# Performance work log

Measured on AMD Instinct MI355X. Metric: run time of the kernel, lower is better.

## Reference

```python
import jax, jax.numpy as jnp
import numpy as np
import math

B, CZ, L = 1, 128, 256
H, C = 4, 32  # num_heads, head dim
EPS = 1e-5


def _conv1x1(w, x):
    # w: (out, in), x: (b, in, i, j) -> (b, out, i, j)
    return jnp.einsum('oc,bcij->boij', w, x)


def setup_inputs() -> dict:
    key = jax.random.key(0)
    ks = jax.random.split(key, 8)
    s = 1.0 / math.sqrt(CZ)
    return {
        'pair_rep': jax.random.normal(ks[0], (B, CZ, L, L), jnp.float32),
        'ln_gamma': jnp.ones((CZ, L, L), jnp.float32),
        'ln_beta': jnp.zeros((CZ, L, L), jnp.float32),
        'w_q': jax.random.normal(ks[1], (H * C, CZ), jnp.float32) * s,
        'w_k': jax.random.normal(ks[2], (H * C, CZ), jnp.float32) * s,
        'w_v': jax.random.normal(ks[3], (H * C, CZ), jnp.float32) * s,
        'w_b': jax.random.normal(ks[4], (H, CZ), jnp.float32) * s,
        'w_g': jax.random.normal(ks[5], (H * C, CZ), jnp.float32) * s,
        'b_g': jnp.zeros((H * C,), jnp.float32),
        'w_rep': jax.random.normal(ks[6], (CZ, H * C), jnp.float32) * s,
        'b_rep': jnp.zeros((CZ,), jnp.float32),
    }


def reference(pair_rep, ln_gamma, ln_beta, w_q, w_k, w_v, w_b, w_g, b_g, w_rep, b_rep):
    # LayerNorm over (c_z, h, w) jointly, full-shape affine (torch LayerNorm([c_z,h,w]))
    mu = jnp.mean(pair_rep, axis=(1, 2, 3), keepdims=True)
    var = jnp.var(pair_rep, axis=(1, 2, 3), keepdims=True)
    x = (pair_rep - mu) * jax.lax.rsqrt(var + EPS) * ln_gamma[None] + ln_beta[None]

    # 1x1 conv projections; channels packed as (h c): channel = h*C + c
    q = _conv1x1(w_q, x).reshape(B, H, C, L, L)  # bhcij
    k = _conv1x1(w_k, x).reshape(B, H, C, L, L)
    v = _conv1x1(w_v, x).reshape(B, H, C, L, L)
    bias = _conv1x1(w_b, x)                       # (b, h, i, j) -> used as bias[b,h,j,k]
    g = jax.nn.sigmoid(_conv1x1(w_g, x) + b_g[None, :, None, None]).reshape(B, H, C, L, L)

    scale = 1.0 / math.sqrt(C)
    # scores[b,h,i,j,k] = scale * sum_c q[b,h,c,i,j] k[b,h,c,i,k] + bias[b,h,j,k]
    scores = scale * jnp.einsum('bhcij,bhcik->bhijk', q, k) + bias[:, :, None, :, :]
    a = jax.nn.softmax(scores, axis=-1)
    # o[b,h,c,i,j] = sum_k a[b,h,i,j,k] v[b,h,c,i,k]  (same math as the 6D broadcast-sum)
    o = g * jnp.einsum('bhijk,bhcik->bhcij', a, v)

    # output repacks channels as (c h): channel = c*H + h
    o = jnp.transpose(o, (0, 2, 1, 3, 4)).reshape(B, C * H, L, L)
    return _conv1x1(w_rep, o) + b_rep[None, :, None, None]
```

## Files before the change

### kernel.cpp

```cpp
#include <hip/hip_runtime.h>
#include <math.h>

#define L 256
#define CZ 128
#define NH 4
#define HD 32
#define P (L*L)
#define NTOT (CZ*P)
#define EPSV 1e-5f
#define SCALE 0.17677669529663687f

typedef unsigned short u16;
typedef _Float16 f16;
typedef __attribute__((ext_vector_type(8))) _Float16 f16x8;
typedef __attribute__((ext_vector_type(4))) _Float16 f16x4;
typedef __attribute__((ext_vector_type(4))) float    f32x4;

__device__ __forceinline__ float bu2f(u16 u){ return __uint_as_float(((unsigned)u) << 16); }
__device__ __forceinline__ u16 f2bu(float x){
  unsigned u = __float_as_uint(x);
  return (u16)((u + 0x7fffu + ((u >> 16) & 1u)) >> 16);
}

template<bool FP32>
__device__ __forceinline__ float ldin(const void* p, size_t i){
  return FP32 ? ((const float*)p)[i] : bu2f(((const u16*)p)[i]);
}
template<bool FP32>
__device__ __forceinline__ void stout(void* p, size_t i, float v){
  if (FP32) ((float*)p)[i] = v; else ((u16*)p)[i] = f2bu(v);
}

__device__ __forceinline__ void glds16(const void* g, void* l){
  __builtin_amdgcn_global_load_lds((const __attribute__((address_space(1))) void*)g,
                                   (__attribute__((address_space(3))) void*)l, 16, 0, 0);
}

#define OFF_WQT   16
#define OFF_WKT   (OFF_WQT+16384)
#define OFF_WVT   (OFF_WKT+16384)
#define OFF_WGT   (OFF_WVT+16384)
#define OFF_WREPT (OFF_WGT+16384)
#define OFF_WBT   (OFF_WREPT+16384)
#define OFF_BGF   (OFF_WBT+512)
#define OFF_BREPF (OFF_BGF+128)
#define OFF_BIAS  (OFF_BREPF+128)
#define OFF_XN    344848
#define OFF_ATTO  (OFF_XN+4194304)
#define WS_NEED   (((size_t)OFF_ATTO + 4194304ull)*4ull)

#define GUARD(ws) if (((((const volatile int*)(ws))[2]) != 0) != FP32) return;

__global__ __launch_bounds__(256) void detect_dtype(const void* pair, int* flag){
  int t = threadIdx.x;
  const u16* u = (const u16*)pair;
  int big = 0;
  for (int k = t; k < 2048; k += 256){
    float av = fabsf(bu2f(u[k]));
    if (!(av < 1e4f)) big = 1;
  }
  __shared__ int sb[256];
  sb[t] = big; __syncthreads();
  for (int off = 128; off > 0; off >>= 1){
    if (t < off) sb[t] |= sb[t+off];
    __syncthreads();
  }
  if (t == 0) flag[2] = sb[0];
}

template<bool FP32>
__global__ __launch_bounds__(256) void prep_w(const void* wq, const void* wk,
    const void* wv, const void* wg, const void* wrep, const void* wb,
    const void* bg, const void* brep, float* ws){
  GUARD(ws);
  int idx = blockIdx.x*256 + threadIdx.x;
  int oc = idx >> 7, cin = idx & 127;
  f16* wf = (f16*)(ws + OFF_WQT);
  wf[0*16384 + idx] = (f16)ldin<FP32>(wq, idx);
  wf[1*16384 + idx] = (f16)ldin<FP32>(wk, idx);
  wf[2*16384 + idx] = (f16)ldin<FP32>(wv, idx);
  wf[3*16384 + idx] = (f16)ldin<FP32>(wg, idx);
  float wr = ldin<FP32>(wrep, idx);
  ws[OFF_WREPT + cin*128 + oc] = wr;
  ((f16*)(ws + OFF_WVT))[oc*128 + (cin&3)*32 + (cin>>2)] = (f16)wr;
  if (idx < 512){ int h = idx >> 7, ci = idx & 127; ws[OFF_WBT + ci*4 + h] = ldin<FP32>(wb, idx); }
  if (idx < 128){ ws[OFF_BGF + idx] = ldin<FP32>(bg, idx); ws[OFF_BREPF + idx] = ldin<FP32>(brep, idx); }
}

template<bool FP32>
__global__ __launch_bounds__(256) void ln_reduce(const void* __restrict__ pair, float* ws){
  GUARD(ws);
  int t = threadIdx.x;
  int g = blockIdx.x*256 + t;
  float s = 0.f, ss = 0.f;
  #pragma unroll
  for (int u = 0; u < 4; ++u){
    size_t vi = (size_t)u*524288 + g;
    if (FP32){
      float4 v = ((const float4*)pair)[vi];
      s += v.x+v.y+v.z+v.w;
      ss += v.x*v.x + v.y*v.y + v.z*v.z + v.w*v.w;
    } else {
      ushort4 v = ((const ushort4*)pair)[vi];
      float a = bu2f(v.x), b = bu2f(v.y), c = bu2f(v.z), d = bu2f(v.w);
      s += a+b+c+d; ss += a*a+b*b+c*c+d*d;
    }
  }
  __shared__ float sa[256], sb[256];
  sa[t] = s; sb[t] = ss;
  __syncthreads();
  for (int off = 128; off > 0; off >>= 1){
    if (t < off){ sa[t] += sa[t+off]; sb[t] += sb[t+off]; }
    __syncthreads();
  }
  if (t == 0){ atomicAdd(&ws[0], sa[0]); atomicAdd(&ws[1], sb[0]); }
}


template<bool FP32>
__global__ __launch_bounds__(256) void xnorm(const void* __restrict__ pair,
    const void* __restrict__ gamma, const void* __restrict__ beta, float* __restrict__ ws){
  GUARD(ws);
  int a = blockIdx.x & 255, q = blockIdx.x >> 8;
  int t = threadIdx.x;
  int cq = t >> 6, b64 = t & 63, j4 = b64 << 2;
  float mu   = ws[0] * (1.0f/NTOT);
  float var  = ws[1] * (1.0f/NTOT) - mu*mu;
  float rstd = rsqrtf(var + EPSV);
  f16 hv[4][8];
  #pragma unroll
  for (int ce = 0; ce < 8; ++ce){
    int c = q*32 + cq*8 + ce;
    size_t vi = (size_t)c*16384 + (size_t)a*64 + b64;
    float p0,p1,p2,p3, g0,g1,g2,g3, e0,e1,e2,e3;
    if (FP32){
      float4 pv = ((const float4*)pair)[vi];
      float4 gv = ((const float4*)gamma)[vi];
      float4 bv = ((const float4*)beta)[vi];
      p0=pv.x;p1=pv.y;p2=pv.z;p3=pv.w; g0=gv.x;g1=gv.y;g2=gv.z;g3=gv.w; e0=bv.x;e1=bv.y;e2=bv.z;e3=bv.w;
    } else {
      ushort4 pv = ((const ushort4*)pair)[vi];
      ushort4 gv = ((const ushort4*)gamma)[vi];
      ushort4 bv = ((const ushort4*)beta)[vi];
      p0=bu2f(pv.x);p1=bu2f(pv.y);p2=bu2f(pv.z);p3=bu2f(pv.w);
      g0=bu2f(gv.x);g1=bu2f(gv.y);g2=bu2f(gv.z);g3=bu2f(gv.w);
      e0=bu2f(bv.x);e1=bu2f(bv.y);e2=bu2f(bv.z);e3=bu2f(bv.w);
    }
    hv[0][ce] = (f16)((p0-mu)*rstd*g0 + e0);
    hv[1][ce] = (f16)((p1-mu)*rstd*g1 + e1);
    hv[2][ce] = (f16)((p2-mu)*rstd*g2 + e2);
    hv[3][ce] = (f16)((p3-mu)*rstd*g3 + e3);
  }
  char* xnb = (char*)ws + (size_t)OFF_XN*4;
  int cb = q*4 + cq;
  #pragma unroll
  for (int col = 0; col < 4; ++col){
    f16x8 v;
    #pragma unroll
    for (int ce = 0; ce < 8; ++ce) v[ce] = hv[col][ce];
    *(f16x8*)(xnb + ((((size_t)a*16 + cb)*256) + (j4+col))*16) = v;
  }
}

__global__ __launch_bounds__(256) void bias_xn(float* __restrict__ ws){
  int a = blockIdx.x & 255, qc = blockIdx.x >> 8, b = threadIdx.x;
  const char* xnb = (const char*)ws + (size_t)OFF_XN*4;
  float a0=0.f, a1=0.f, a2=0.f, a3=0.f;
  #pragma unroll
  for (int cc = 0; cc < 4; ++cc){
    int cb = qc*4 + cc;
    f16x8 v = *(const f16x8*)(xnb + ((((size_t)a*16 + cb)*256) + b)*16);
    #pragma unroll
    for (int ce = 0; ce < 8; ++ce){
      int c = cb*8 + ce;
      float xv = (float)v[ce];
      const float* w4 = ws + OFF_WBT + c*4;
      a0 = fmaf(w4[0], xv, a0); a1 = fmaf(w4[1], xv, a1);
      a2 = fmaf(w4[2], xv, a2); a3 = fmaf(w4[3], xv, a3);
    }
  }
  atomicAdd(&ws[OFF_BIAS + 0*P + a*L + b], a0);
  atomicAdd(&ws[OFF_BIAS + 1*P + a*L + b], a1);
  atomicAdd(&ws[OFF_BIAS + 2*P + a*L + b], a2);
  atomicAdd(&ws[OFF_BIAS + 3*P + a*L + b], a3);
}

__global__ __launch_bounds__(256, 4) void attn_xn(float* __restrict__ ws){
  __shared__ __align__(16) char smem[32768];
  char* Ab = smem;
  char* Bb = smem + 16384;
  const int t = threadIdx.x;
  int bid = blockIdx.x;
  int sw = ((bid & 7) << 7) | (bid >> 3);
  const int h = sw >> 8, i = sw & 255;
  const int w = t >> 6, l = t & 63;
  const int l15 = l & 15, l4 = l >> 4;
  const char* xnb = (const char*)ws + (size_t)OFF_XN*4 + (size_t)i*65536;
  const f16* wf = (const f16*)(ws + OFF_WQT);

  auto stage = [&](int q){
    #pragma unroll
    for (int cbl = 0; cbl < 4; ++cbl){
      int jsrc = (w*64 + l) ^ cbl;
      const char* src = xnb + (size_t)((q*4 + cbl)*4096) + (size_t)jsrc*16;
      glds16(src, Ab + cbl*4096 + w*1024);
    }
  };

  f32x4 acc[2][4][2];
  auto projpass = [&](int pr0){
    #pragma unroll
    for (int pp = 0; pp < 2; ++pp)
      #pragma unroll
      for (int mj = 0; mj < 4; ++mj)
        #pragma unroll
        for (int nt = 0; nt < 2; ++nt) acc[pp][mj][nt] = f32x4{0.f,0.f,0.f,0.f};
    #pragma unroll
    for (int q = 0; q < 4; ++q){
      __syncthreads();
      f16x8 A[4];
      #pragma unroll
      for (int mj = 0; mj < 4; ++mj){
        int j = 64*w + 16*mj + l15;
        A[mj] = *(const f16x8*)(Ab + l4*4096 + ((j ^ l4)*16));
      }
      __syncthreads();
      if (q < 3) stage(q+1);
      #pragma unroll
      for (int pp = 0; pp < 2; ++pp){
        #pragma unroll
        for (int nt = 0; nt < 2; ++nt){
          int o = h*32 + nt*16 + l15;
          f16x8 Bf = *(const f16x8*)(wf + (pr0+pp)*16384 + o*128 + q*32 + 8*l4);
          #pragma unroll
          for (int mj = 0; mj < 4; ++mj)
            acc[pp][mj][nt] = __builtin_amdgcn_mfma_f32_16x16x32_f16(A[mj], Bf, acc[pp][mj][nt], 0, 0, 0);
        }
      }
    }
  };

  stage(0);
  projpass(0);
  __syncthreads();
  stage(0);
  #pragma unroll
  for (int mj = 0; mj < 4; ++mj){
    #pragma unroll
    for (int nt = 0; nt < 2; ++nt){
      int ob = 2*nt + (l15 >> 3), oe = l15 & 7;
      int kb4 = 64*w + 16*mj + 4*l4;
      #pragma unroll
      for (int r = 0; r < 4; ++r)
        *(f16*)(Bb + ((ob*4096 + (kb4+r)*16 + oe*2) ^ ((ob&3)<<4))) = (f16)acc[0][mj][nt][r];
    }
  }
  __syncthreads();
  f16x8 qa[4];
  #pragma unroll
  for (int mj = 0; mj < 4; ++mj){
    int j = 64*w + 16*mj + l15;
    qa[mj] = *(const f16x8*)(Bb + ((l4*4096 + j*16) ^ ((l4&3)<<4)));
  }
  __syncthreads();
  #pragma unroll
  for (int mj = 0; mj < 4; ++mj){
    #pragma unroll
    for (int nt = 0; nt < 2; ++nt){
      int ob = 2*nt + (l15 >> 3), oe = l15 & 7;
      int kb4 = 64*w + 16*mj + 4*l4;
      #pragma unroll
      for (int r = 0; r < 4; ++r)
        *(f16*)(Bb + ((ob*4096 + (kb4+r)*16 + oe*2) ^ ((ob&3)<<4))) = (f16)acc[1][mj][nt][r];
    }
  }

  projpass(2);
  f16x4 gsh[4][2];
  #pragma unroll
  for (int mj = 0; mj < 4; ++mj){
    #pragma unroll
    for (int nt = 0; nt < 2; ++nt){
      float bgv = ws[OFF_BGF + h*32 + nt*16 + l15];
      #pragma unroll
      for (int r = 0; r < 4; ++r){
        float z = acc[1][mj][nt][r] + bgv;
        gsh[mj][nt][r] = (f16)(1.0f/(1.0f + __expf(-z)));
      }
    }
  }
  __syncthreads();
  #pragma unroll
  for (int mj = 0; mj < 4; ++mj){
    #pragma unroll
    for (int nt = 0; nt < 2; ++nt){
      int c = nt*16 + l15;
      int kkq = 16*w + 4*mj + l4;
      f16x4 pv;
      #pragma unroll
      for (int r = 0; r < 4; ++r) pv[r] = (f16)acc[0][mj][nt][r];
      *(f16x4*)(Ab + kkq*256 + ((c*8) ^ (l4<<3))) = pv;
    }
  }
  __syncthreads();

  f32x4 oacc[4][2];
  #pragma unroll
  for (int mj = 0; mj < 4; ++mj)
    #pragma unroll
    for (int nt = 0; nt < 2; ++nt) oacc[mj][nt] = f32x4{0.f,0.f,0.f,0.f};
  float lp[4] = {0.f,0.f,0.f,0.f};
  const float* bias2 = ws + OFF_BIAS + (size_t)h*P;
  const f32x4 zz = {0.f,0.f,0.f,0.f};

  for (int kt = 0; kt < 8; ++kt){
    int kk0 = kt*32, kkq0 = kt*8;
    f16x8 kbf[2];
    #pragma unroll
    for (int tt = 0; tt < 2; ++tt)
      kbf[tt] = *(const f16x8*)(Bb + ((l4*4096 + (kk0+16*tt+l15)*16) ^ ((l4&3)<<4)));
    f16x4 vb[2][2];
    #pragma unroll
    for (int tt = 0; tt < 2; ++tt)
      #pragma unroll
      for (int nt = 0; nt < 2; ++nt)
        vb[tt][nt] = *(const f16x4*)(Ab + (kkq0+4*tt+l4)*256 + ((((l15+16*nt)*8)) ^ (l4<<3)));
    #pragma unroll
    for (int mj = 0; mj < 4; ++mj){
      int j = 64*w + 16*mj + l15;
      const float* bp = bias2 + (size_t)j*256 + kk0 + 4*l4;
      #pragma unroll
      for (int tt = 0; tt < 2; ++tt){
        f32x4 s = __builtin_amdgcn_mfma_f32_16x16x32_f16(kbf[tt], qa[mj], zz, 0, 0, 0);
        float4 bv = *(const float4*)(bp + 16*tt);
        f16x4 pa;
        {
          float e0 = __expf(fmaf(s[0], SCALE, bv.x - 4.0f));
          float e1 = __expf(fmaf(s[1], SCALE, bv.y - 4.0f));
          float e2 = __expf(fmaf(s[2], SCALE, bv.z - 4.0f));
          float e3 = __expf(fmaf(s[3], SCALE, bv.w - 4.0f));
          lp[mj] += (e0+e1)+(e2+e3);
          pa[0]=(f16)e0; pa[1]=(f16)e1; pa[2]=(f16)e2; pa[3]=(f16)e3;
        }
        #pragma unroll
        for (int nt = 0; nt < 2; ++nt)
          oacc[mj][nt] = __builtin_amdgcn_mfma_f32_16x16x16f16(pa, vb[tt][nt], oacc[mj][nt], 0, 0, 0);
      }
    }
  }

  float inv[4];
  #pragma unroll
  for (int mj = 0; mj < 4; ++mj){
    float v = lp[mj];
    v += __shfl_xor(v, 16);
    v += __shfl_xor(v, 32);
    inv[mj] = 1.0f / v;
  }
  __syncthreads();
  #pragma unroll
  for (int mj = 0; mj < 4; ++mj){
    #pragma unroll
    for (int r = 0; r < 4; ++r){
      float iv = __shfl(inv[mj], 20*l4 + r);
      int j = 64*w + 16*mj + 4*l4 + r;
      #pragma unroll
      for (int nt = 0; nt < 2; ++nt){
        int c = nt*16 + l15;
        float ov = oacc[mj][nt][r] * iv * (float)gsh[mj][nt][r];
        *(f16*)(Bb + c*512 + ((j*2) ^ ((c&7)<<4))) = (f16)ov;
      }
    }
  }
  __syncthreads();
  char* ao = (char*)ws + (size_t)OFF_ATTO*4;
  #pragma unroll
  for (int cb8 = 0; cb8 < 4; ++cb8){
    f16x8 v;
    #pragma unroll
    for (int e = 0; e < 8; ++e){
      int c = cb8*8 + e;
      v[e] = *(const f16*)(Bb + c*512 + ((t*2) ^ ((c&7)<<4)));
    }
    *(f16x8*)(ao + (((size_t)i*256 + t)*128 + h*32)*2 + cb8*16) = v;
  }
}

template<bool FP32>
__global__ __launch_bounds__(256, 4) void out_proj_mf(float* __restrict__ ws, void* __restrict__ outp){
  GUARD(ws);
  __shared__ __align__(16) char smem[32768];
  char* Ab = smem;
  char* Ob = smem + 16384;
  const int t = threadIdx.x;
  int bid = blockIdx.x;
  int sw2 = ((bid & 7) << 6) | (bid >> 3);
  const int oh = sw2 >> 8, i = sw2 & 255;
  const int w = t >> 6, l = t & 63;
  const int l15 = l & 15, l4 = l >> 4;
  const char* aob = (const char*)ws + (size_t)OFF_ATTO*4 + (size_t)i*65536;
  const f16* w2 = (const f16*)(ws + OFF_WVT);

  auto stage = [&](int q){
    #pragma unroll
    for (int cbl = 0; cbl < 4; ++cbl){
      int jsrc = (w*64 + l) ^ cbl;
      const char* src = aob + (size_t)jsrc*256 + (q*4 + cbl)*16;
      glds16(src, Ab + cbl*4096 + w*1024);
    }
  };

  f32x4 acc[4][4];
  #pragma unroll
  for (int nt = 0; nt < 4; ++nt)
    #pragma unroll
    for (int mj = 0; mj < 4; ++mj) acc[nt][mj] = f32x4{0.f,0.f,0.f,0.f};

  stage(0);
  #pragma unroll
  for (int q = 0; q < 4; ++q){
    __syncthreads();
    f16x8 A[4];
    #pragma unroll
    for (int mj = 0; mj < 4; ++mj){
      int j = 64*w + 16*mj + l15;
      A[mj] = *(const f16x8*)(Ab + l4*4096 + ((j ^ l4)*16));
    }
    __syncthreads();
    if (q < 3) stage(q+1);
    #pragma unroll
    for (int nt = 0; nt < 4; ++nt){
      int oc = oh*64 + nt*16 + l15;
      f16x8 Bf = *(const f16x8*)(w2 + oc*128 + q*32 + 8*l4);
      #pragma unroll
      for (int mj = 0; mj < 4; ++mj)
        acc[nt][mj] = __builtin_amdgcn_mfma_f32_16x16x32_f16(A[mj], Bf, acc[nt][mj], 0, 0, 0);
    }
  }
  #pragma unroll
  for (int nt = 0; nt < 4; ++nt){
    __syncthreads();
    #pragma unroll
    for (int mj = 0; mj < 4; ++mj){
      #pragma unroll
      for (int r = 0; r < 4; ++r){
        int j = 64*w + 16*mj + 4*l4 + r;
        *(float*)(Ob + l15*1024 + ((j*4) ^ ((l15&7)<<4))) = acc[nt][mj][r];
      }
    }
    __syncthreads();
    #pragma unroll
    for (int o2 = 0; o2 < 16; ++o2){
      int oc = oh*64 + nt*16 + o2;
      float v = *(const float*)(Ob + o2*1024 + ((t*4) ^ ((o2&7)<<4)));
      stout<FP32>(outp, (size_t)oc*P + (size_t)i*L + t, v + ws[OFF_BREPF + oc]);
    }
  }
}


template<bool FP32>
__global__ __launch_bounds__(256) void bias_old(const void* __restrict__ pair,
    const void* __restrict__ gamma, const void* __restrict__ beta, float* __restrict__ ws){
  GUARD(ws);
  int a = blockIdx.x & 255, q = blockIdx.x >> 8, b = threadIdx.x;
  float mu   = ws[0] * (1.0f/NTOT);
  float var  = ws[1] * (1.0f/NTOT) - mu*mu;
  float rstd = rsqrtf(var + EPSV);
  float a0=0.f, a1=0.f, a2=0.f, a3=0.f;
  int c0 = q*32;
  for (int cc = 0; cc < 32; ++cc){
    int c = c0 + cc;
    size_t idx = (size_t)c*P + (size_t)a*L + b;
    float xv = (ldin<FP32>(pair,idx) - mu)*rstd*ldin<FP32>(gamma,idx) + ldin<FP32>(beta,idx);
    const float* w4 = ws + OFF_WBT + c*4;
    a0 = fmaf(w4[0], xv, a0); a1 = fmaf(w4[1], xv, a1);
    a2 = fmaf(w4[2], xv, a2); a3 = fmaf(w4[3], xv, a3);
  }
  atomicAdd(&ws[OFF_BIAS + 0*P + a*L + b], a0);
  atomicAdd(&ws[OFF_BIAS + 1*P + a*L + b], a1);
  atomicAdd(&ws[OFF_BIAS + 2*P + a*L + b], a2);
  atomicAdd(&ws[OFF_BIAS + 3*P + a*L + b], a3);
}

template<bool FP32>
__global__ __launch_bounds__(256, 2) void attn_old(const void* __restrict__ pair,
    const void* __restrict__ gamma, const void* __restrict__ beta,
    float* __restrict__ ws, void* __restrict__ outp){
  GUARD(ws);
  __shared__ __align__(16) char smem[65536];
  char* Ab  = smem;
  char* KTb = smem + 32768;
  char* V2b = smem + 49152;
  const int t = threadIdx.x;
  const int h = blockIdx.x >> 8, i = blockIdx.x & 255;
  const int w = t >> 6, l = t & 63;
  const int l15 = l & 15, l4 = l >> 4;
  const float mu   = ws[0] * (1.0f/NTOT);
  const float var  = ws[1] * (1.0f/NTOT) - mu*mu;
  const float rstd = rsqrtf(var + EPSV);
  const f16* wf = (const f16*)(ws + OFF_WQT);
  f32x4 acc[4][4][2];
  #pragma unroll
  for (int pr=0;pr<4;++pr)
    #pragma unroll
    for(int mj=0;mj<4;++mj)
      #pragma unroll
      for(int nt=0;nt<2;++nt) acc[pr][mj][nt] = f32x4{0.f,0.f,0.f,0.f};
  for (int half = 0; half < 2; ++half){
    #pragma unroll
    for (int cb = 0; cb < 8; ++cb){
      int cc0 = cb*8;
      f16x8 hv;
      #pragma unroll
      for (int e = 0; e < 8; ++e){
        size_t idx = (size_t)(half*64 + cc0 + e)*P + (size_t)i*L + t;
        float xv = (ldin<FP32>(pair,idx) - mu)*rstd*ldin<FP32>(gamma,idx) + ldin<FP32>(beta,idx);
        hv[e] = (f16)xv;
      }
      *(f16x8*)(Ab + t*128 + ((cc0*2) ^ ((t&7)<<4))) = hv;
    }
    __syncthreads();
    #pragma unroll
    for (int ksl = 0; ksl < 2; ++ksl){
      int cin0 = half*64 + ksl*32;
      f16x8 A[4];
      #pragma unroll
      for (int mj = 0; mj < 4; ++mj){
        int j = 64*w + 16*mj + l15;
        A[mj] = *(const f16x8*)(Ab + j*128 + (((ksl*32 + 8*l4)*2) ^ ((j&7)<<4)));
      }
      #pragma unroll
      for (int pr = 0; pr < 4; ++pr){
        #pragma unroll
        for (int nt = 0; nt < 2; ++nt){
          int o = h*32 + nt*16 + l15;
          f16x8 Bf = *(const f16x8*)(wf + pr*16384 + o*128 + cin0 + 8*l4);
          #pragma unroll
          for (int mj = 0; mj < 4; ++mj)
            acc[pr][mj][nt] = __builtin_amdgcn_mfma_f32_16x16x32_f16(A[mj], Bf, acc[pr][mj][nt], 0, 0, 0);
        }
      }
    }
    __syncthreads();
  }
  f32x4 gs[4][2];
  #pragma unroll
  for (int mj = 0; mj < 4; ++mj){
    #pragma unroll
    for (int nt = 0; nt < 2; ++nt){
      float bgv = ws[OFF_BGF + h*32 + nt*16 + l15];
      #pragma unroll
      for (int r = 0; r < 4; ++r){
        float z = acc[3][mj][nt][r] + bgv;
        gs[mj][nt][r] = 1.0f/(1.0f + __expf(-z));
      }
    }
  }
  #pragma unroll
  for (int mj = 0; mj < 4; ++mj){
    #pragma unroll
    for (int nt = 0; nt < 2; ++nt){
      int o = nt*16 + l15;
      int kb4 = 64*w + 16*mj + 4*l4;
      f16x4 pv;
      #pragma unroll
      for (int r = 0; r < 4; ++r){
        int j = kb4 + r;
        *(f16*)(Ab  + j*64 + ((o*2) ^ ((j&3)<<4))) = (f16)acc[0][mj][nt][r];
        *(f16*)(KTb + j*64 + ((o*2) ^ ((j&3)<<4))) = (f16)acc[1][mj][nt][r];
        pv[r] = (f16)acc[2][mj][nt][r];
      }
      *(f16x4*)(V2b + o*512 + ((kb4*2) ^ ((o&7)<<4))) = pv;
    }
  }
  __syncthreads();
  f16x8 qa[4];
  #pragma unroll
  for (int mj = 0; mj < 4; ++mj){
    int j = 64*w + 16*mj + l15;
    qa[mj] = *(const f16x8*)(Ab + j*64 + ((16*l4) ^ ((j&3)<<4)));
  }
  __syncthreads();
  f32x4 oacc[4][2];
  #pragma unroll
  for (int mj=0;mj<4;++mj)
    #pragma unroll
    for(int nt=0;nt<2;++nt) oacc[mj][nt] = f32x4{0.f,0.f,0.f,0.f};
  float lp[16];
  #pragma unroll
  for (int u = 0; u < 16; ++u) lp[u] = 0.f;
  const float* bias2 = ws + OFF_BIAS + (size_t)h*P;
  const f32x4 zz = {0.f,0.f,0.f,0.f};
  for (int kt = 0; kt < 4; ++kt){
    int kk0 = kt*64;
    #pragma unroll
    for (int nk = 0; nk < 4; ++nk){
      int kkr = kk0 + nk*16 + l15;
      f16x8 kbf = *(const f16x8*)(KTb + kkr*64 + ((16*l4) ^ ((kkr&3)<<4)));
      #pragma unroll
      for (int mj = 0; mj < 4; ++mj){
        f32x4 s = __builtin_amdgcn_mfma_f32_16x16x32_f16(qa[mj], kbf, zz, 0, 0, 0);
        #pragma unroll
        for (int r = 0; r < 4; ++r){
          int j = 64*w + 16*mj + 4*l4 + r;
          float bv = bias2[(size_t)j*L + kkr] - 4.0f;
          float e = __expf(fmaf(s[r], SCALE, bv));
          lp[mj*4+r] += e;
          *(f16*)(Ab + j*128 + (((nk*16+l15)*2) ^ ((j&7)<<4))) = (f16)e;
        }
      }
    }
    __syncthreads();
    #pragma unroll
    for (int ks2 = 0; ks2 < 2; ++ks2){
      f16x8 vb[2];
      #pragma unroll
      for (int nt = 0; nt < 2; ++nt){
        int c = nt*16 + l15;
        vb[nt] = *(const f16x8*)(V2b + c*512 + (((kk0 + ks2*32 + 8*l4)*2) ^ ((c&7)<<4)));
      }
      #pragma unroll
      for (int mj = 0; mj < 4; ++mj){
        int j = 64*w + 16*mj + l15;
        f16x8 pa = *(const f16x8*)(Ab + j*128 + (((ks2*32 + 8*l4)*2) ^ ((j&7)<<4)));
        #pragma unroll
        for (int nt = 0; nt < 2; ++nt)
          oacc[mj][nt] = __builtin_amdgcn_mfma_f32_16x16x32_f16(pa, vb[nt], oacc[mj][nt], 0, 0, 0);
      }
    }
  }
  __syncthreads();
  #pragma unroll
  for (int u = 0; u < 16; ++u){
    float v = lp[u];
    v += __shfl_xor(v, 1);
    v += __shfl_xor(v, 2);
    v += __shfl_xor(v, 4);
    v += __shfl_xor(v, 8);
    lp[u] = 1.0f / v;
  }
  #pragma unroll
  for (int mj = 0; mj < 4; ++mj){
    #pragma unroll
    for (int nt = 0; nt < 2; ++nt){
      int c = nt*16 + l15;
      #pragma unroll
      for (int r = 0; r < 4; ++r){
        int j = 64*w + 16*mj + 4*l4 + r;
        float ov = oacc[mj][nt][r] * lp[mj*4+r] * gs[mj][nt][r];
        *(float*)(Ab + c*1024 + ((j*4) ^ ((c&7)<<4))) = ov;
      }
    }
  }
  __syncthreads();
  #pragma unroll
  for (int c = 0; c < 32; ++c){
    float v = *(const float*)(Ab + c*1024 + ((t*4) ^ ((c&7)<<4)));
    stout<FP32>(outp, (size_t)(c*NH + h)*P + (size_t)i*L + t, v);
  }
}

template<bool FP32>
__global__ __launch_bounds__(256) void out_proj_old(float* __restrict__ ws, void* __restrict__ outp){
  GUARD(ws);
  __shared__ float gos[CZ*65];
  int blk = blockIdx.x;
  int i = blk >> 2, jb = (blk & 3) << 6;
  int t = threadIdx.x;
  for (int u = 0; u < 32; ++u){
    int lin = u*256 + t;
    int m = lin >> 6, p = lin & 63;
    gos[m*65 + p] = ldin<FP32>(outp, (size_t)m*P + (size_t)i*L + jb + p);
  }
  __syncthreads();
  int p = t & 63, w4 = t >> 6;
  int woc = w4*32;
  float acc[32];
  #pragma unroll
  for (int o = 0; o < 32; ++o) acc[o] = 0.f;
  for (int cin = 0; cin < CZ; ++cin){
    float xv = gos[cin*65 + p];
    const float* wrow = ws + OFF_WREPT + cin*128 + woc;
    #pragma unroll
    for (int o = 0; o < 32; ++o) acc[o] = fmaf(wrow[o], xv, acc[o]);
  }
  #pragma unroll
  for (int o = 0; o < 32; ++o){
    int oc = woc + o;
    stout<FP32>(outp, (size_t)oc*P + (size_t)i*L + jb + p, acc[o] + ws[OFF_BREPF + oc]);
  }
}

extern "C" void kernel_launch(void* const* d_in, const int* in_sizes, int n_in,
                              void* d_out, int out_size, void* d_ws, size_t ws_size,
                              hipStream_t stream) {
  (void)in_sizes; (void)n_in; (void)out_size;
  const void* pair  = d_in[0];
  const void* gamma = d_in[1];
  const void* beta  = d_in[2];
  const void* wq    = d_in[3];
  const void* wk    = d_in[4];
  const void* wv    = d_in[5];
  const void* wb    = d_in[6];
  const void* wg    = d_in[7];
  const void* bg    = d_in[8];
  const void* wrep  = d_in[9];
  const void* brep  = d_in[10];
  float* ws = (float*)d_ws;
  bool big = ws_size >= WS_NEED;

  hipMemsetAsync(d_ws, 0, 16, stream);
  hipMemsetAsync((char*)d_ws + (size_t)OFF_BIAS*4, 0, (size_t)NH*P*4, stream);
  detect_dtype<<<1, 256, 0, stream>>>(pair, (int*)d_ws);

  prep_w<false>   <<<64,   256, 0, stream>>>(wq, wk, wv, wg, wrep, wb, bg, brep, ws);
  prep_w<true>    <<<64,   256, 0, stream>>>(wq, wk, wv, wg, wrep, wb, bg, brep, ws);
  ln_reduce<false><<<2048, 256, 0, stream>>>(pair, ws);
  ln_reduce<true> <<<2048, 256, 0, stream>>>(pair, ws);

  if (big){
    xnorm<false>       <<<1024, 256, 0, stream>>>(pair, gamma, beta, ws);
    xnorm<true>        <<<1024, 256, 0, stream>>>(pair, gamma, beta, ws);
    bias_xn            <<<1024, 256, 0, stream>>>(ws);
    attn_xn            <<<1024, 256, 0, stream>>>(ws);
    out_proj_mf<false> <<<512,  256, 0, stream>>>(ws, d_out);
    out_proj_mf<true>  <<<512,  256, 0, stream>>>(ws, d_out);
  } else {
    bias_old<false>    <<<1024, 256, 0, stream>>>(pair, gamma, beta, ws);
    bias_old<true>     <<<1024, 256, 0, stream>>>(pair, gamma, beta, ws);
    attn_old<false>    <<<1024, 256, 0, stream>>>(pair, gamma, beta, ws, d_out);
    attn_old<true>     <<<1024, 256, 0, stream>>>(pair, gamma, beta, ws, d_out);
    out_proj_old<false><<<1024, 256, 0, stream>>>(ws, d_out);
    out_proj_old<true> <<<1024, 256, 0, stream>>>(ws, d_out);
  }
}
```

Before: 330.3 us.

## Fuse bias projection into xnorm, drop dual-dtype launches, relayout attention output

The separate bias_xn pass is folded into xnorm: each block accumulates the per-head bias projection from fp32 normalized values, reduces it through shared memory and atomically adds it, with the softmax offset of -4 folded into the stored bias instead of being applied in attn_xn. The templated FP32/BF16 kernel pairs, which each launched twice and returned early on a guard, become single kernels that branch on the runtime dtype flag, removing several launches. attn_xn now preloads bias tiles ahead of the MFMA loop, and the attention output is stored head-major so out_proj_mf can stage it contiguously. out_proj_mf uses 1024 blocks of 32 output channels instead of 512 blocks of 64, trading weight and A-tile reuse for more parallelism.

```diff
diff --git a/kernel.cpp b/kernel.cpp
--- a/kernel.cpp
+++ b/kernel.cpp
@@ -22,6 +22,12 @@
   return (u16)((u + 0x7fffu + ((u >> 16) & 1u)) >> 16);
 }
 
+__device__ __forceinline__ float ldr(bool fp32, const void* p, size_t i){
+  return fp32 ? ((const float*)p)[i] : bu2f(((const u16*)p)[i]);
+}
+__device__ __forceinline__ void str(bool fp32, void* p, size_t i, float v){
+  if (fp32) ((float*)p)[i] = v; else ((u16*)p)[i] = f2bu(v);
+}
 template<bool FP32>
 __device__ __forceinline__ float ldin(const void* p, size_t i){
   return FP32 ? ((const float*)p)[i] : bu2f(((const u16*)p)[i]);
@@ -50,6 +56,7 @@
 #define WS_NEED   (((size_t)OFF_ATTO + 4194304ull)*4ull)
 
 #define GUARD(ws) if (((((const volatile int*)(ws))[2]) != 0) != FP32) return;
+#define RFLAG(ws) (((const volatile int*)(ws))[2] != 0)
 
 __global__ __launch_bounds__(256) void detect_dtype(const void* pair, int* flag){
   int t = threadIdx.x;
@@ -68,40 +75,40 @@
   if (t == 0) flag[2] = sb[0];
 }
 
-template<bool FP32>
 __global__ __launch_bounds__(256) void prep_w(const void* wq, const void* wk,
     const void* wv, const void* wg, const void* wrep, const void* wb,
     const void* bg, const void* brep, float* ws){
-  GUARD(ws);
+  bool fp32 = RFLAG(ws);
   int idx = blockIdx.x*256 + threadIdx.x;
   int oc = idx >> 7, cin = idx & 127;
   f16* wf = (f16*)(ws + OFF_WQT);
-  wf[0*16384 + idx] = (f16)ldin<FP32>(wq, idx);
-  wf[1*16384 + idx] = (f16)ldin<FP32>(wk, idx);
-  wf[2*16384 + idx] = (f16)ldin<FP32>(wv, idx);
-  wf[3*16384 + idx] = (f16)ldin<FP32>(wg, idx);
-  float wr = ldin<FP32>(wrep, idx);
+  wf[0*16384 + idx] = (f16)ldr(fp32, wq, idx);
+  wf[1*16384 + idx] = (f16)ldr(fp32, wk, idx);
+  wf[2*16384 + idx] = (f16)ldr(fp32, wv, idx);
+  wf[3*16384 + idx] = (f16)ldr(fp32, wg, idx);
+  float wr = ldr(fp32, wrep, idx);
   ws[OFF_WREPT + cin*128 + oc] = wr;
   ((f16*)(ws + OFF_WVT))[oc*128 + (cin&3)*32 + (cin>>2)] = (f16)wr;
-  if (idx < 512){ int h = idx >> 7, ci = idx & 127; ws[OFF_WBT + ci*4 + h] = ldin<FP32>(wb, idx); }
-  if (idx < 128){ ws[OFF_BGF + idx] = ldin<FP32>(bg, idx); ws[OFF_BREPF + idx] = ldin<FP32>(brep, idx); }
-}
-
-template<bool FP32>
+  if (idx < 512){ int h = idx >> 7, ci = idx & 127; ws[OFF_WBT + ci*4 + h] = ldr(fp32, wb, idx); }
+  if (idx < 128){ ws[OFF_BGF + idx] = ldr(fp32, bg, idx); ws[OFF_BREPF + idx] = ldr(fp32, brep, idx); }
+}
+
 __global__ __launch_bounds__(256) void ln_reduce(const void* __restrict__ pair, float* ws){
-  GUARD(ws);
+  bool fp32 = RFLAG(ws);
   int t = threadIdx.x;
   int g = blockIdx.x*256 + t;
   float s = 0.f, ss = 0.f;
-  #pragma unroll
-  for (int u = 0; u < 4; ++u){
-    size_t vi = (size_t)u*524288 + g;
-    if (FP32){
-      float4 v = ((const float4*)pair)[vi];
+  if (fp32){
+    #pragma unroll
+    for (int u = 0; u < 4; ++u){
+      float4 v = ((const float4*)pair)[(size_t)u*524288 + g];
       s += v.x+v.y+v.z+v.w;
       ss += v.x*v.x + v.y*v.y + v.z*v.z + v.w*v.w;
-    } else {
-      ushort4 v = ((const ushort4*)pair)[vi];
+    }
+  } else {
+    #pragma unroll
+    for (int u = 0; u < 4; ++u){
+      ushort4 v = ((const ushort4*)pair)[(size_t)u*524288 + g];
       float a = bu2f(v.x), b = bu2f(v.y), c = bu2f(v.z), d = bu2f(v.w);
       s += a+b+c+d; ss += a*a+b*b+c*c+d*d;
     }
@@ -117,10 +124,9 @@
 }
 
 
-template<bool FP32>
 __global__ __launch_bounds__(256) void xnorm(const void* __restrict__ pair,
     const void* __restrict__ gamma, const void* __restrict__ beta, float* __restrict__ ws){
-  GUARD(ws);
+  bool fp32 = RFLAG(ws);
   int a = blockIdx.x & 255, q = blockIdx.x >> 8;
   int t = threadIdx.x;
   int cq = t >> 6, b64 = t & 63, j4 = b64 << 2;
@@ -128,12 +134,17 @@
   float var  = ws[1] * (1.0f/NTOT) - mu*mu;
   float rstd = rsqrtf(var + EPSV);
   f16 hv[4][8];
+  float pb[4][4];
+  #pragma unroll
+  for (int col = 0; col < 4; ++col)
+    #pragma unroll
+    for (int h = 0; h < 4; ++h) pb[col][h] = 0.f;
   #pragma unroll
   for (int ce = 0; ce < 8; ++ce){
     int c = q*32 + cq*8 + ce;
     size_t vi = (size_t)c*16384 + (size_t)a*64 + b64;
     float p0,p1,p2,p3, g0,g1,g2,g3, e0,e1,e2,e3;
-    if (FP32){
+    if (fp32){
       float4 pv = ((const float4*)pair)[vi];
       float4 gv = ((const float4*)gamma)[vi];
       float4 bv = ((const float4*)beta)[vi];
@@ -146,10 +157,20 @@
       g0=bu2f(gv.x);g1=bu2f(gv.y);g2=bu2f(gv.z);g3=bu2f(gv.w);
       e0=bu2f(bv.x);e1=bu2f(bv.y);e2=bu2f(bv.z);e3=bu2f(bv.w);
     }
-    hv[0][ce] = (f16)((p0-mu)*rstd*g0 + e0);
-    hv[1][ce] = (f16)((p1-mu)*rstd*g1 + e1);
-    hv[2][ce] = (f16)((p2-mu)*rstd*g2 + e2);
-    hv[3][ce] = (f16)((p3-mu)*rstd*g3 + e3);
+    float x0 = (p0-mu)*rstd*g0 + e0;
+    float x1 = (p1-mu)*rstd*g1 + e1;
+    float x2 = (p2-mu)*rstd*g2 + e2;
+    float x3 = (p3-mu)*rstd*g3 + e3;
+    hv[0][ce] = (f16)x0; hv[1][ce] = (f16)x1; hv[2][ce] = (f16)x2; hv[3][ce] = (f16)x3;
+    float4 w4 = *(const float4*)(ws + OFF_WBT + c*4);
+    pb[0][0] = fmaf(w4.x, x0, pb[0][0]); pb[0][1] = fmaf(w4.y, x0, pb[0][1]);
+    pb[0][2] = fmaf(w4.z, x0, pb[0][2]); pb[0][3] = fmaf(w4.w, x0, pb[0][3]);
+    pb[1][0] = fmaf(w4.x, x1, pb[1][0]); pb[1][1] = fmaf(w4.y, x1, pb[1][1]);
+    pb[1][2] = fmaf(w4.z, x1, pb[1][2]); pb[1][3] = fmaf(w4.w, x1, pb[1][3]);
+    pb[2][0] = fmaf(w4.x, x2, pb[2][0]); pb[2][1] = fmaf(w4.y, x2, pb[2][1]);
+    pb[2][2] = fmaf(w4.z, x2, pb[2][2]); pb[2][3] = fmaf(w4.w, x2, pb[2][3]);
+    pb[3][0] = fmaf(w4.x, x3, pb[3][0]); pb[3][1] = fmaf(w4.y, x3, pb[3][1]);
+    pb[3][2] = fmaf(w4.z, x3, pb[3][2]); pb[3][3] = fmaf(w4.w, x3, pb[3][3]);
   }
   char* xnb = (char*)ws + (size_t)OFF_XN*4;
   int cb = q*4 + cq;
@@ -160,29 +181,20 @@
     for (int ce = 0; ce < 8; ++ce) v[ce] = hv[col][ce];
     *(f16x8*)(xnb + ((((size_t)a*16 + cb)*256) + (j4+col))*16) = v;
   }
-}
-
-__global__ __launch_bounds__(256) void bias_xn(float* __restrict__ ws){
-  int a = blockIdx.x & 255, qc = blockIdx.x >> 8, b = threadIdx.x;
-  const char* xnb = (const char*)ws + (size_t)OFF_XN*4;
-  float a0=0.f, a1=0.f, a2=0.f, a3=0.f;
-  #pragma unroll
-  for (int cc = 0; cc < 4; ++cc){
-    int cb = qc*4 + cc;
-    f16x8 v = *(const f16x8*)(xnb + ((((size_t)a*16 + cb)*256) + b)*16);
-    #pragma unroll
-    for (int ce = 0; ce < 8; ++ce){
-      int c = cb*8 + ce;
-      float xv = (float)v[ce];
-      const float* w4 = ws + OFF_WBT + c*4;
-      a0 = fmaf(w4[0], xv, a0); a1 = fmaf(w4[1], xv, a1);
-      a2 = fmaf(w4[2], xv, a2); a3 = fmaf(w4[3], xv, a3);
-    }
-  }
-  atomicAdd(&ws[OFF_BIAS + 0*P + a*L + b], a0);
-  atomicAdd(&ws[OFF_BIAS + 1*P + a*L + b], a1);
-  atomicAdd(&ws[OFF_BIAS + 2*P + a*L + b], a2);
-  atomicAdd(&ws[OFF_BIAS + 3*P + a*L + b], a3);
+  __shared__ float sbb[4][64][16];
+  #pragma unroll
+  for (int col = 0; col < 4; ++col)
+    #pragma unroll
+    for (int h = 0; h < 4; ++h) sbb[cq][b64][h*4+col] = pb[col][h];
+  __syncthreads();
+  #pragma unroll
+  for (int k = 0; k < 4; ++k){
+    int lin = k*256 + t;
+    int bb = lin >> 4, hc = lin & 15;
+    float v = sbb[0][bb][hc] + sbb[1][bb][hc] + sbb[2][bb][hc] + sbb[3][bb][hc];
+    int h = hc >> 2, col = hc & 3;
+    atomicAdd(&ws[OFF_BIAS + h*P + a*256 + bb*4 + col], v - 1.0f);
+  }
 }
 
 __global__ __launch_bounds__(256, 4) void attn_xn(float* __restrict__ ws){
@@ -315,6 +327,13 @@
 
   for (int kt = 0; kt < 8; ++kt){
     int kk0 = kt*32, kkq0 = kt*8;
+    float4 bvv[4][2];
+    #pragma unroll
+    for (int mj = 0; mj < 4; ++mj){
+      const float* bp = bias2 + (size_t)(64*w + 16*mj + l15)*256 + kk0 + 4*l4;
+      bvv[mj][0] = *(const float4*)bp;
+      bvv[mj][1] = *(const float4*)(bp + 16);
+    }
     f16x8 kbf[2];
     #pragma unroll
     for (int tt = 0; tt < 2; ++tt)
@@ -327,18 +346,16 @@
         vb[tt][nt] = *(const f16x4*)(Ab + (kkq0+4*tt+l4)*256 + ((((l15+16*nt)*8)) ^ (l4<<3)));
     #pragma unroll
     for (int mj = 0; mj < 4; ++mj){
-      int j = 64*w + 16*mj + l15;
-      const float* bp = bias2 + (size_t)j*256 + kk0 + 4*l4;
       #pragma unroll
       for (int tt = 0; tt < 2; ++tt){
         f32x4 s = __builtin_amdgcn_mfma_f32_16x16x32_f16(kbf[tt], qa[mj], zz, 0, 0, 0);
-        float4 bv = *(const float4*)(bp + 16*tt);
+        float4 bv = bvv[mj][tt];
         f16x4 pa;
         {
-          float e0 = __expf(fmaf(s[0], SCALE, bv.x - 4.0f));
-          float e1 = __expf(fmaf(s[1], SCALE, bv.y - 4.0f));
-          float e2 = __expf(fmaf(s[2], SCALE, bv.z - 4.0f));
-          float e3 = __expf(fmaf(s[3], SCALE, bv.w - 4.0f));
+          float e0 = __expf(fmaf(s[0], SCALE, bv.x));
+          float e1 = __expf(fmaf(s[1], SCALE, bv.y));
+          float e2 = __expf(fmaf(s[2], SCALE, bv.z));
+          float e3 = __expf(fmaf(s[3], SCALE, bv.w));
           lp[mj] += (e0+e1)+(e2+e3);
           pa[0]=(f16)e0; pa[1]=(f16)e1; pa[2]=(f16)e2; pa[3]=(f16)e3;
         }
@@ -373,7 +390,7 @@
     }
   }
   __syncthreads();
-  char* ao = (char*)ws + (size_t)OFF_ATTO*4;
+  char* ao = (char*)ws + (size_t)OFF_ATTO*4 + (size_t)h*4194304 + ((size_t)i*256)*64;
   #pragma unroll
   for (int cb8 = 0; cb8 < 4; ++cb8){
     f16x8 v;
@@ -382,37 +399,36 @@
       int c = cb8*8 + e;
       v[e] = *(const f16*)(Bb + c*512 + ((t*2) ^ ((c&7)<<4)));
     }
-    *(f16x8*)(ao + (((size_t)i*256 + t)*128 + h*32)*2 + cb8*16) = v;
-  }
-}
-
-template<bool FP32>
+    *(f16x8*)(ao + (size_t)t*64 + cb8*16) = v;
+  }
+}
+
 __global__ __launch_bounds__(256, 4) void out_proj_mf(float* __restrict__ ws, void* __restrict__ outp){
-  GUARD(ws);
+  bool fp32 = RFLAG(ws);
   __shared__ __align__(16) char smem[32768];
   char* Ab = smem;
   char* Ob = smem + 16384;
   const int t = threadIdx.x;
   int bid = blockIdx.x;
-  int sw2 = ((bid & 7) << 6) | (bid >> 3);
+  int sw2 = ((bid & 7) << 7) | (bid >> 3);
   const int oh = sw2 >> 8, i = sw2 & 255;
   const int w = t >> 6, l = t & 63;
   const int l15 = l & 15, l4 = l >> 4;
-  const char* aob = (const char*)ws + (size_t)OFF_ATTO*4 + (size_t)i*65536;
+  const char* aob = (const char*)ws + (size_t)OFF_ATTO*4;
   const f16* w2 = (const f16*)(ws + OFF_WVT);
 
   auto stage = [&](int q){
     #pragma unroll
     for (int cbl = 0; cbl < 4; ++cbl){
       int jsrc = (w*64 + l) ^ cbl;
-      const char* src = aob + (size_t)jsrc*256 + (q*4 + cbl)*16;
+      const char* src = aob + (size_t)q*4194304 + ((size_t)i*256 + jsrc)*64 + cbl*16;
       glds16(src, Ab + cbl*4096 + w*1024);
     }
   };
 
-  f32x4 acc[4][4];
-  #pragma unroll
-  for (int nt = 0; nt < 4; ++nt)
+  f32x4 acc[2][4];
+  #pragma unroll
+  for (int nt = 0; nt < 2; ++nt)
     #pragma unroll
     for (int mj = 0; mj < 4; ++mj) acc[nt][mj] = f32x4{0.f,0.f,0.f,0.f};
 
@@ -429,8 +445,8 @@
     __syncthreads();
     if (q < 3) stage(q+1);
     #pragma unroll
-    for (int nt = 0; nt < 4; ++nt){
-      int oc = oh*64 + nt*16 + l15;
+    for (int nt = 0; nt < 2; ++nt){
+      int oc = oh*32 + nt*16 + l15;
       f16x8 Bf = *(const f16x8*)(w2 + oc*128 + q*32 + 8*l4);
       #pragma unroll
       for (int mj = 0; mj < 4; ++mj)
@@ -438,7 +454,7 @@
     }
   }
   #pragma unroll
-  for (int nt = 0; nt < 4; ++nt){
+  for (int nt = 0; nt < 2; ++nt){
     __syncthreads();
     #pragma unroll
     for (int mj = 0; mj < 4; ++mj){
@@ -451,9 +467,9 @@
     __syncthreads();
     #pragma unroll
     for (int o2 = 0; o2 < 16; ++o2){
-      int oc = oh*64 + nt*16 + o2;
+      int oc = oh*32 + nt*16 + o2;
       float v = *(const float*)(Ob + o2*1024 + ((t*4) ^ ((o2&7)<<4)));
-      stout<FP32>(outp, (size_t)oc*P + (size_t)i*L + t, v + ws[OFF_BREPF + oc]);
+      str(fp32, outp, (size_t)oc*P + (size_t)i*L + t, v + ws[OFF_BREPF + oc]);
     }
   }
 }
@@ -714,18 +730,13 @@
   hipMemsetAsync((char*)d_ws + (size_t)OFF_BIAS*4, 0, (size_t)NH*P*4, stream);
   detect_dtype<<<1, 256, 0, stream>>>(pair, (int*)d_ws);
 
-  prep_w<false>   <<<64,   256, 0, stream>>>(wq, wk, wv, wg, wrep, wb, bg, brep, ws);
-  prep_w<true>    <<<64,   256, 0, stream>>>(wq, wk, wv, wg, wrep, wb, bg, brep, ws);
-  ln_reduce<false><<<2048, 256, 0, stream>>>(pair, ws);
-  ln_reduce<true> <<<2048, 256, 0, stream>>>(pair, ws);
+  prep_w   <<<64,   256, 0, stream>>>(wq, wk, wv, wg, wrep, wb, bg, brep, ws);
+  ln_reduce<<<2048, 256, 0, stream>>>(pair, ws);
 
   if (big){
-    xnorm<false>       <<<1024, 256, 0, stream>>>(pair, gamma, beta, ws);
-    xnorm<true>        <<<1024, 256, 0, stream>>>(pair, gamma, beta, ws);
-    bias_xn            <<<1024, 256, 0, stream>>>(ws);
-    attn_xn            <<<1024, 256, 0, stream>>>(ws);
-    out_proj_mf<false> <<<512,  256, 0, stream>>>(ws, d_out);
-    out_proj_mf<true>  <<<512,  256, 0, stream>>>(ws, d_out);
+    xnorm      <<<1024, 256, 0, stream>>>(pair, gamma, beta, ws);
+    attn_xn    <<<1024, 256, 0, stream>>>(ws);
+    out_proj_mf<<<1024, 256, 0, stream>>>(ws, d_out);
   } else {
     bias_old<false>    <<<1024, 256, 0, stream>>>(pair, gamma, beta, ws);
     bias_old<true>     <<<1024, 256, 0, stream>>>(pair, gamma, beta, ws);
```

New measurement: 317.4 us. 3.9% less time.
